# Performance work log

Hardware: AMD Instinct MI355X
Metric: run time of the kernel (lower is better)

The kernel has to match this reference:

```python
import jax, jax.numpy as jnp
import numpy as np

B, T, C, H = 2, 2048, 768, 12
HD = C // H  # head dim = 64


def setup_inputs() -> dict:
    key = jax.random.key(0)
    k1, k2, k3 = jax.random.split(key, 3)
    s_in = 1.0 / np.sqrt(C)
    return {
        "x": jax.random.normal(k1, (B, T, C), dtype=jnp.float32),
        "Wqkv": jax.random.normal(k2, (C, 3 * C), dtype=jnp.float32) * s_in,
        "bqkv": jnp.zeros((3 * C,), dtype=jnp.float32),
        "Wproj": jax.random.normal(k3, (C, C), dtype=jnp.float32) * s_in,
        "bproj": jnp.zeros((C,), dtype=jnp.float32),
    }


def reference(x, Wqkv, bqkv, Wproj, bproj):
    b, t, c = x.shape
    qkv = x @ Wqkv + bqkv                      # [b, t, 3c]
    q, k, v = jnp.split(qkv, 3, axis=2)
    # [b, h, t, hd]
    q = q.reshape(b, t, H, HD).transpose(0, 2, 1, 3)
    k = k.reshape(b, t, H, HD).transpose(0, 2, 1, 3)
    v = v.reshape(b, t, H, HD).transpose(0, 2, 1, 3)
    scale = 1.0 / np.sqrt(HD)
    att = jnp.einsum("bhqd,bhkd->bhqk", q, k) * scale  # [b, h, t, t]
    causal = jnp.tril(jnp.ones((t, t), dtype=bool))
    att = jnp.where(causal[None, None], att, -jnp.inf)
    att = jax.nn.softmax(att, axis=-1)
    y = jnp.einsum("bhqk,bhkd->bhqd", att, v)          # [b, h, t, hd]
    y = y.transpose(0, 2, 1, 3).reshape(b, t, c)
    return y @ Wproj + bproj
```

## Files before the change

### kernel.cpp

```cpp
#include <hip/hip_runtime.h>
#include <math.h>

#define BB 2
#define TT 2048
#define CC 768
#define HH 12
#define HD 64
#define N3 (3*CC)

typedef __attribute__((ext_vector_type(8))) short short8;
typedef __attribute__((ext_vector_type(8))) _Float16 f16x8;
typedef __attribute__((ext_vector_type(4))) float f32x4;
typedef unsigned short u16;

#define QSCALE 0.1803368809f

static __device__ __forceinline__ u16 f2h(float x) {
    union { _Float16 h; u16 u; } v; v.h = (_Float16)x; return v.u;
}
static __device__ __forceinline__ float ex2(float x) {
#if __has_builtin(__builtin_amdgcn_exp2f)
    return __builtin_amdgcn_exp2f(x);
#else
    return exp2f(x);
#endif
}
static __device__ __forceinline__ unsigned pk2h(float a, float b) {
    auto p = __builtin_amdgcn_cvt_pkrtz(a, b);
    return __builtin_bit_cast(unsigned, p);
}

static __device__ __forceinline__ void gl16(const void* g, void* l) {
    __builtin_amdgcn_global_load_lds(
        (const __attribute__((address_space(1))) void*)g,
        (__attribute__((address_space(3))) void*)l, 16, 0, 0);
}

__global__ __launch_bounds__(256)
void conv_h(const float* __restrict__ src, u16* __restrict__ dst)
{
    const int i = blockIdx.x * 256 + threadIdx.x;
    float4 v = ((const float4*)src)[i];
    ushort4 o;
    o.x = f2h(v.x); o.y = f2h(v.y); o.z = f2h(v.z); o.w = f2h(v.w);
    ((ushort4*)dst)[i] = o;
}

__global__ __launch_bounds__(256)
void conv_th(const float* __restrict__ W, u16* __restrict__ Th, int N)
{
    __shared__ float Tt[64][65];
    const int tid = threadIdx.x;
    const int n0 = blockIdx.x * 64, k0 = blockIdx.y * 64;
    {
        const int r = tid >> 2, q = tid & 3;
        #pragma unroll
        for (int i = 0; i < 4; ++i) {
            float4 v = *(const float4*)(W + (size_t)(k0 + r) * N + n0 + q * 16 + i * 4);
            Tt[q * 16 + i * 4 + 0][r] = v.x;
            Tt[q * 16 + i * 4 + 1][r] = v.y;
            Tt[q * 16 + i * 4 + 2][r] = v.z;
            Tt[q * 16 + i * 4 + 3][r] = v.w;
        }
    }
    __syncthreads();
    {
        const int n = tid >> 2, q = tid & 3;
        u16 hh[16];
        #pragma unroll
        for (int j = 0; j < 16; ++j) hh[j] = f2h(Tt[n][q * 16 + j]);
        u16* dh = Th + (size_t)(n0 + n) * 768 + k0 + q * 16;
        *(short8*)(dh) = *(short8*)&hh[0];
        *(short8*)(dh + 8) = *(short8*)&hh[8];
    }
}

template<int NCOLS, int MODE>
__global__ __launch_bounds__(256)
void mm3(const u16* __restrict__ A_g, const u16* __restrict__ B_g,
         const float* __restrict__ bias, float* __restrict__ outF,
         u16* __restrict__ qo, u16* __restrict__ ko, u16* __restrict__ vto)
{
    __shared__ u16 gsm[16384];
    char* smb = (char*)gsm;
    const int tid = threadIdx.x, lane = tid & 63, wv = tid >> 6;
    const int wm = wv >> 1, wn = wv & 1, r16 = lane & 15, kg = lane >> 4;
    const int m0 = blockIdx.y * 128, n0 = blockIdx.x * 128;

    const u16 *pA[2], *pB[2];
    int ldsq[2];
    #pragma unroll
    for (int qq = 0; qq < 2; ++qq) {
        const int L = wv * 2048 + qq * 1024 + lane * 16;
        const int row = L >> 6, c = (L >> 4) & 3;
        const int cp = c ^ ((row >> 1) & 3);
        ldsq[qq] = wv * 2048 + qq * 1024;
        pA[qq] = A_g + (size_t)(m0 + row) * 768 + cp * 8;
        pB[qq] = B_g + (size_t)(n0 + row) * 768 + cp * 8;
    }

    int aA[4], aB[4];
    #pragma unroll
    for (int t = 0; t < 4; ++t) {
        const int rA = wm * 64 + t * 16 + r16;
        const int rB = wn * 64 + t * 16 + r16;
        aA[t] = rA * 64 + ((kg ^ ((rA >> 1) & 3)) << 4);
        aB[t] = rB * 64 + ((kg ^ ((rB >> 1) & 3)) << 4) + 8192;
    }

    f32x4 acc[4][4];
    #pragma unroll
    for (int i = 0; i < 4; ++i)
        #pragma unroll
        for (int j = 0; j < 4; ++j) acc[i][j] = (f32x4)0.f;

    #pragma unroll
    for (int qq = 0; qq < 2; ++qq) {
        gl16(pA[qq], smb + ldsq[qq]);
        gl16(pB[qq], smb + 8192 + ldsq[qq]);
        pA[qq] += 32; pB[qq] += 32;
    }
    __syncthreads();

    int cur = 0;
    for (int ks = 0; ks < 24; ++ks) {
        const int nxt = cur ^ 1;
        if (ks != 23) {
            #pragma unroll
            for (int qq = 0; qq < 2; ++qq) {
                gl16(pA[qq], smb + nxt * 16384 + ldsq[qq]);
                gl16(pB[qq], smb + nxt * 16384 + 8192 + ldsq[qq]);
                pA[qq] += 32; pB[qq] += 32;
            }
        }
        const int cb = cur * 16384;
        f16x8 a[4], b[4];
        #pragma unroll
        for (int t = 0; t < 4; ++t) {
            a[t] = *(const f16x8*)(smb + cb + aA[t]);
            b[t] = *(const f16x8*)(smb + cb + aB[t]);
        }
        #pragma unroll
        for (int mt = 0; mt < 4; ++mt)
            #pragma unroll
            for (int nt = 0; nt < 4; ++nt)
                acc[mt][nt] = __builtin_amdgcn_mfma_f32_16x16x32_f16(a[mt], b[nt], acc[mt][nt], 0, 0, 0);
        __syncthreads();
        cur = nxt;
    }

    float bi[4];
    #pragma unroll
    for (int nt = 0; nt < 4; ++nt) bi[nt] = bias[n0 + wn * 64 + nt * 16 + r16];

    if (MODE == 1) {
        #pragma unroll
        for (int mt = 0; mt < 4; ++mt)
            #pragma unroll
            for (int nt = 0; nt < 4; ++nt)
                #pragma unroll
                for (int r = 0; r < 4; ++r) {
                    const int grow = m0 + wm * 64 + mt * 16 + kg * 4 + r;
                    const int gcol = n0 + wn * 64 + nt * 16 + r16;
                    outF[(size_t)grow * CC + gcol] = acc[mt][nt][r] + bi[nt];
                }
    } else {
        const int which = n0 / CC;
        const float qsc = (which == 0) ? QSCALE : 1.0f;
        const int b_ = m0 >> 11;
        #pragma unroll
        for (int mt = 0; mt < 4; ++mt) {
            const int tb = ((m0 & 2047) + wm * 64 + mt * 16 + kg * 4);
            #pragma unroll
            for (int nt = 0; nt < 4; ++nt) {
                const int gcol = n0 + wn * 64 + nt * 16 + r16;
                const int cc = gcol - which * CC;
                const int h = cc >> 6, d = cc & 63;
                const int bh_ = b_ * HH + h;
                if (which == 2) {
                    ushort4 hv;
                    #pragma unroll
                    for (int r = 0; r < 4; ++r)
                        ((u16*)&hv)[r] = f2h(acc[mt][nt][r] + bi[nt]);
                    *(ushort4*)(vto + ((size_t)bh_ * 64 + d) * 2048 + tb) = hv;
                } else {
                    u16* dst = (which == 0) ? qo : ko;
                    #pragma unroll
                    for (int r = 0; r < 4; ++r)
                        dst[(((size_t)bh_ * 2048 + tb + r) << 6) + d] =
                            f2h((acc[mt][nt][r] + bi[nt]) * qsc);
                }
            }
        }
    }
}

__global__ __launch_bounds__(256)
void attn3(const u16* __restrict__ qp, const u16* __restrict__ kp,
           const u16* __restrict__ vtp, u16* __restrict__ attp)
{
    __shared__ u16 smem[20480];
    char* smb = (char*)smem;

    const int tid = threadIdx.x, bid = blockIdx.x;
    const int qt = 31 - (bid / 24);
    const int bh = bid % 24;
    const int lane = tid & 63, wv = tid >> 6;
    const int r16 = lane & 15, kg = lane >> 4;
    const int r7 = r16 & 7;

    const size_t qro = ((size_t)bh * TT + qt * 64 + wv * 16 + r16) * 64;
    f16x8 qf[2];
    #pragma unroll
    for (int ks = 0; ks < 2; ++ks)
        qf[ks] = *(const f16x8*)(qp + qro + ks * 32 + kg * 8);

    const u16 *pk[2], *pv[2];
    int ldsq[2];
    #pragma unroll
    for (int qq = 0; qq < 2; ++qq) {
        const int L = wv * 2048 + qq * 1024 + lane * 16;
        const int row = L >> 7, c = (L >> 4) & 7;
        const int cp = c ^ (row & 7);
        ldsq[qq] = wv * 2048 + qq * 1024;
        pk[qq] = kp + ((size_t)bh * TT + row) * 64 + cp * 8;
        pv[qq] = vtp + ((size_t)bh * 64 + row) * TT + cp * 8;
    }

    int aK[2][4], aP[2];
    #pragma unroll
    for (int ks = 0; ks < 2; ++ks) {
        #pragma unroll
        for (int nt = 0; nt < 4; ++nt) {
            const int row = nt * 16 + r16;
            aK[ks][nt] = row * 128 + (((ks * 4 + kg) ^ (row & 7)) << 4);
        }
        aP[ks] = 32768 + wv * 2048 + r16 * 128 + (((ks * 4 + kg) ^ r7) << 4);
    }
    const int pwbase = 32768 + wv * 2048 + r16 * 128;
    const int kg8 = kg * 8, kg4 = kg * 4;

    f32x4 o_acc[4];
    #pragma unroll
    for (int i = 0; i < 4; ++i) o_acc[i] = (f32x4)0.f;
    f32x4 o_l = (f32x4)0.f;
    float m = -1e30f;

    f16x8 ones;
    #pragma unroll
    for (int i = 0; i < 8; ++i) ones[i] = (_Float16)1.0f;

    #pragma unroll
    for (int qq = 0; qq < 2; ++qq) {
        gl16(pk[qq], smb + ldsq[qq]);
        gl16(pv[qq], smb + 8192 + ldsq[qq]);
        pk[qq] += 4096; pv[qq] += 64;
    }
    __syncthreads();

    int cur = 0;
    for (int j = 0; j <= qt; ++j) {
        const int nxt = cur ^ 1;
        if (j != qt) {
            #pragma unroll
            for (int qq = 0; qq < 2; ++qq) {
                gl16(pk[qq], smb + nxt * 16384 + ldsq[qq]);
                gl16(pv[qq], smb + nxt * 16384 + 8192 + ldsq[qq]);
                pk[qq] += 4096; pv[qq] += 64;
            }
        }
        const int cb = cur * 16384;

        f32x4 s[4];
        #pragma unroll
        for (int nt = 0; nt < 4; ++nt) s[nt] = (f32x4)0.f;
        __builtin_amdgcn_s_setprio(1);
        #pragma unroll
        for (int ks = 0; ks < 2; ++ks)
            #pragma unroll
            for (int nt = 0; nt < 4; ++nt) {
                f16x8 kf = *(const f16x8*)(smb + cb + aK[ks][nt]);
                s[nt] = __builtin_amdgcn_mfma_f32_16x16x32_f16(kf, qf[ks], s[nt], 0, 0, 0);
            }
        __builtin_amdgcn_s_setprio(0);

        if (j == qt) {
            #pragma unroll
            for (int nt = 0; nt < 4; ++nt)
                #pragma unroll
                for (int r = 0; r < 4; ++r)
                    if (nt * 16 + kg4 + r > wv * 16 + r16) s[nt][r] = -1e30f;
        }

        float pm = s[0][0];
        #pragma unroll
        for (int nt = 0; nt < 4; ++nt)
            #pragma unroll
            for (int r = 0; r < 4; ++r)
                if (nt | r) pm = fmaxf(pm, s[nt][r]);
        pm = fmaxf(pm, __shfl_xor(pm, 16));
        pm = fmaxf(pm, __shfl_xor(pm, 32));

        if (__any(pm > m + 8.0f)) {
            const float mn = fmaxf(m, pm);
            const float corr = ex2(m - mn);
            m = mn;
            const float c0 = __shfl(corr, kg4 + 0);
            const float c1 = __shfl(corr, kg4 + 1);
            const float c2 = __shfl(corr, kg4 + 2);
            const float c3 = __shfl(corr, kg4 + 3);
            #pragma unroll
            for (int nt = 0; nt < 4; ++nt) {
                o_acc[nt][0] *= c0; o_acc[nt][1] *= c1;
                o_acc[nt][2] *= c2; o_acc[nt][3] *= c3;
            }
            o_l[0] *= c0; o_l[1] *= c1; o_l[2] *= c2; o_l[3] *= c3;
        }

        #pragma unroll
        for (int nt = 0; nt < 4; ++nt) {
            const float p0 = ex2(s[nt][0] - m), p1 = ex2(s[nt][1] - m);
            const float p2 = ex2(s[nt][2] - m), p3 = ex2(s[nt][3] - m);
            uint2 w;
            w.x = pk2h(p0, p1);
            w.y = pk2h(p2, p3);
            *(uint2*)(smb + pwbase + ((nt * 32 + kg8) ^ (r7 << 4))) = w;
        }

        __builtin_amdgcn_s_setprio(1);
        #pragma unroll
        for (int ks = 0; ks < 2; ++ks) {
            f16x8 pa = *(const f16x8*)(smb + aP[ks]);
            o_l = __builtin_amdgcn_mfma_f32_16x16x32_f16(pa, ones, o_l, 0, 0, 0);
            #pragma unroll
            for (int nt = 0; nt < 4; ++nt) {
                f16x8 vf = *(const f16x8*)(smb + cb + 8192 + aK[ks][nt]);
                o_acc[nt] = __builtin_amdgcn_mfma_f32_16x16x32_f16(pa, vf, o_acc[nt], 0, 0, 0);
            }
        }
        __builtin_amdgcn_s_setprio(0);

        __syncthreads();
        cur = nxt;
    }

    const int b_ = bh / HH, h = bh % HH;
    #pragma unroll
    for (int r = 0; r < 4; ++r) {
        const float inv = 1.f / o_l[r];
        const int t = qt * 64 + wv * 16 + kg4 + r;
        const size_t base = ((size_t)b_ * TT + t) * CC + h * 64;
        #pragma unroll
        for (int nt = 0; nt < 4; ++nt)
            attp[base + nt * 16 + r16] = f2h(o_acc[nt][r] * inv);
    }
}

extern "C" void kernel_launch(void* const* d_in, const int* in_sizes, int n_in,
                              void* d_out, int out_size, void* d_ws, size_t ws_size,
                              hipStream_t stream)
{
    const float* x     = (const float*)d_in[0];
    const float* Wqkv  = (const float*)d_in[1];
    const float* bqkv  = (const float*)d_in[2];
    const float* Wproj = (const float*)d_in[3];
    const float* bproj = (const float*)d_in[4];
    float* out = (float*)d_out;

    const size_t E  = (size_t)4096 * 768;
    const size_t WQ = (size_t)2304 * 768;
    const size_t WP = (size_t)768 * 768;

    u16* ws   = (u16*)d_ws;
    u16* xh   = ws;
    u16* atth = ws;
    u16* wqh  = ws + E;
    u16* wph  = wqh + WQ;
    u16* qh   = wph + WP;
    u16* kh   = qh + E;
    u16* vth  = kh + E;

    conv_h<<<dim3((int)(E / 4 / 256)), 256, 0, stream>>>(x, xh);
    conv_th<<<dim3(N3 / 64, CC / 64), 256, 0, stream>>>(Wqkv, wqh, N3);
    conv_th<<<dim3(CC / 64, CC / 64), 256, 0, stream>>>(Wproj, wph, CC);

    mm3<N3, 0><<<dim3(N3 / 128, 32), 256, 0, stream>>>(
        xh, wqh, bqkv, nullptr, qh, kh, vth);
    attn3<<<dim3(768), 256, 0, stream>>>(qh, kh, vth, atth);
    mm3<CC, 1><<<dim3(CC / 128, 32), 256, 0, stream>>>(
        atth, wph, bproj, out, nullptr, nullptr, nullptr);
}
```

Measured before the change: 156.2 us.

## Process two query tiles per attention block and merge conversion kernels

```diff
diff --git a/kernel.cpp b/kernel.cpp
--- a/kernel.cpp
+++ b/kernel.cpp
@@ -37,21 +37,26 @@
 }
 
 __global__ __launch_bounds__(256)
-void conv_h(const float* __restrict__ src, u16* __restrict__ dst)
-{
-    const int i = blockIdx.x * 256 + threadIdx.x;
-    float4 v = ((const float4*)src)[i];
-    ushort4 o;
-    o.x = f2h(v.x); o.y = f2h(v.y); o.z = f2h(v.z); o.w = f2h(v.w);
-    ((ushort4*)dst)[i] = o;
-}
-
-__global__ __launch_bounds__(256)
-void conv_th(const float* __restrict__ W, u16* __restrict__ Th, int N)
+void conv_all(const float* __restrict__ x, u16* __restrict__ xh,
+              const float* __restrict__ Wq, u16* __restrict__ wqh,
+              const float* __restrict__ Wp, u16* __restrict__ wph)
 {
     __shared__ float Tt[64][65];
+    const int b = blockIdx.x;
+    if (b < 3072) {
+        const int i = b * 256 + threadIdx.x;
+        float4 v = ((const float4*)x)[i];
+        ushort4 o;
+        o.x = f2h(v.x); o.y = f2h(v.y); o.z = f2h(v.z); o.w = f2h(v.w);
+        ((ushort4*)xh)[i] = o;
+        return;
+    }
+    const float* W; u16* T; int N, idx;
+    if (b < 3504) { W = Wq; T = wqh; N = N3; idx = b - 3072; }
+    else          { W = Wp; T = wph; N = CC; idx = b - 3504; }
+    const int ntx = N / 64;
+    const int n0 = (idx % ntx) * 64, k0 = (idx / ntx) * 64;
     const int tid = threadIdx.x;
-    const int n0 = blockIdx.x * 64, k0 = blockIdx.y * 64;
     {
         const int r = tid >> 2, q = tid & 3;
         #pragma unroll
@@ -69,7 +74,7 @@
         u16 hh[16];
         #pragma unroll
         for (int j = 0; j < 16; ++j) hh[j] = f2h(Tt[n][q * 16 + j]);
-        u16* dh = Th + (size_t)(n0 + n) * 768 + k0 + q * 16;
+        u16* dh = T + (size_t)(n0 + n) * 768 + k0 + q * 16;
         *(short8*)(dh) = *(short8*)&hh[0];
         *(short8*)(dh + 8) = *(short8*)&hh[8];
     }
@@ -199,21 +204,29 @@
 void attn3(const u16* __restrict__ qp, const u16* __restrict__ kp,
            const u16* __restrict__ vtp, u16* __restrict__ attp)
 {
-    __shared__ u16 smem[20480];
+    __shared__ u16 smem[24576];
     char* smb = (char*)smem;
 
     const int tid = threadIdx.x, bid = blockIdx.x;
-    const int qt = 31 - (bid / 24);
+    const int qt = 15 - (bid / 24);
     const int bh = bid % 24;
+    const int t0 = qt * 128;
+    const int jmax = 2 * qt + 1;
+    const int diagA = 2 * qt;
     const int lane = tid & 63, wv = tid >> 6;
     const int r16 = lane & 15, kg = lane >> 4;
     const int r7 = r16 & 7;
-
-    const size_t qro = ((size_t)bh * TT + qt * 64 + wv * 16 + r16) * 64;
-    f16x8 qf[2];
-    #pragma unroll
-    for (int ks = 0; ks < 2; ++ks)
-        qf[ks] = *(const f16x8*)(qp + qro + ks * 32 + kg * 8);
+    const int kg8 = kg * 8, kg4 = kg * 4;
+
+    const size_t qroA = ((size_t)bh * TT + t0 + wv * 16 + r16) * 64;
+    f16x8 qfA[2], qfB[2];
+    #pragma unroll
+    for (int ks = 0; ks < 2; ++ks) {
+        qfA[ks] = *(const f16x8*)(qp + qroA + ks * 32 + kg8);
+        qfB[ks] = *(const f16x8*)(qp + qroA + 4096 + ks * 32 + kg8);
+    }
+    const int rowA = t0 + wv * 16 + r16;
+    const int rowB = rowA + 64;
 
     const u16 *pk[2], *pv[2];
     int ldsq[2];
@@ -227,7 +240,7 @@
         pv[qq] = vtp + ((size_t)bh * 64 + row) * TT + cp * 8;
     }
 
-    int aK[2][4], aP[2];
+    int aK[2][4], aPA[2], aPB[2];
     #pragma unroll
     for (int ks = 0; ks < 2; ++ks) {
         #pragma unroll
@@ -235,16 +248,17 @@
             const int row = nt * 16 + r16;
             aK[ks][nt] = row * 128 + (((ks * 4 + kg) ^ (row & 7)) << 4);
         }
-        aP[ks] = 32768 + wv * 2048 + r16 * 128 + (((ks * 4 + kg) ^ r7) << 4);
-    }
-    const int pwbase = 32768 + wv * 2048 + r16 * 128;
-    const int kg8 = kg * 8, kg4 = kg * 4;
-
-    f32x4 o_acc[4];
-    #pragma unroll
-    for (int i = 0; i < 4; ++i) o_acc[i] = (f32x4)0.f;
-    f32x4 o_l = (f32x4)0.f;
-    float m = -1e30f;
+        aPA[ks] = 32768 + wv * 2048 + r16 * 128 + (((ks * 4 + kg) ^ r7) << 4);
+        aPB[ks] = aPA[ks] + 8192;
+    }
+    const int pwA = 32768 + wv * 2048 + r16 * 128;
+    const int pwB = pwA + 8192;
+
+    f32x4 oA[4], oB[4];
+    #pragma unroll
+    for (int i = 0; i < 4; ++i) { oA[i] = (f32x4)0.f; oB[i] = (f32x4)0.f; }
+    f32x4 lA = (f32x4)0.f, lB = (f32x4)0.f;
+    float mA = -1e30f, mB = -1e30f;
 
     f16x8 ones;
     #pragma unroll
@@ -259,9 +273,9 @@
     __syncthreads();
 
     int cur = 0;
-    for (int j = 0; j <= qt; ++j) {
+    for (int j = 0; j <= jmax; ++j) {
         const int nxt = cur ^ 1;
-        if (j != qt) {
+        if (j != jmax) {
             #pragma unroll
             for (int qq = 0; qq < 2; ++qq) {
                 gl16(pk[qq], smb + nxt * 16384 + ldsq[qq]);
@@ -270,72 +284,87 @@
             }
         }
         const int cb = cur * 16384;
-
-        f32x4 s[4];
-        #pragma unroll
-        for (int nt = 0; nt < 4; ++nt) s[nt] = (f32x4)0.f;
+        const int kb = j * 64;
+
+        f32x4 sA[4], sB[4];
+        #pragma unroll
+        for (int nt = 0; nt < 4; ++nt) { sA[nt] = (f32x4)0.f; sB[nt] = (f32x4)0.f; }
         __builtin_amdgcn_s_setprio(1);
         #pragma unroll
         for (int ks = 0; ks < 2; ++ks)
             #pragma unroll
             for (int nt = 0; nt < 4; ++nt) {
                 f16x8 kf = *(const f16x8*)(smb + cb + aK[ks][nt]);
-                s[nt] = __builtin_amdgcn_mfma_f32_16x16x32_f16(kf, qf[ks], s[nt], 0, 0, 0);
+                sA[nt] = __builtin_amdgcn_mfma_f32_16x16x32_f16(kf, qfA[ks], sA[nt], 0, 0, 0);
+                sB[nt] = __builtin_amdgcn_mfma_f32_16x16x32_f16(kf, qfB[ks], sB[nt], 0, 0, 0);
             }
         __builtin_amdgcn_s_setprio(0);
 
-        if (j == qt) {
+        if (j >= diagA) {
             #pragma unroll
             for (int nt = 0; nt < 4; ++nt)
                 #pragma unroll
                 for (int r = 0; r < 4; ++r)
-                    if (nt * 16 + kg4 + r > wv * 16 + r16) s[nt][r] = -1e30f;
-        }
-
-        float pm = s[0][0];
-        #pragma unroll
-        for (int nt = 0; nt < 4; ++nt)
-            #pragma unroll
-            for (int r = 0; r < 4; ++r)
-                if (nt | r) pm = fmaxf(pm, s[nt][r]);
-        pm = fmaxf(pm, __shfl_xor(pm, 16));
-        pm = fmaxf(pm, __shfl_xor(pm, 32));
-
-        if (__any(pm > m + 8.0f)) {
-            const float mn = fmaxf(m, pm);
-            const float corr = ex2(m - mn);
-            m = mn;
-            const float c0 = __shfl(corr, kg4 + 0);
-            const float c1 = __shfl(corr, kg4 + 1);
-            const float c2 = __shfl(corr, kg4 + 2);
-            const float c3 = __shfl(corr, kg4 + 3);
+                    if (kb + nt * 16 + kg4 + r > rowA) sA[nt][r] = -1e30f;
+        }
+        if (j == jmax) {
+            #pragma unroll
+            for (int nt = 0; nt < 4; ++nt)
+                #pragma unroll
+                for (int r = 0; r < 4; ++r)
+                    if (kb + nt * 16 + kg4 + r > rowB) sB[nt][r] = -1e30f;
+        }
+
+        auto softmax = [&](f32x4 (&s)[4], float& m, f32x4& ol, f32x4 (&oa)[4],
+                           int pwbase) {
+            float pm = s[0][0];
+            #pragma unroll
+            for (int nt = 0; nt < 4; ++nt)
+                #pragma unroll
+                for (int r = 0; r < 4; ++r)
+                    if (nt | r) pm = fmaxf(pm, s[nt][r]);
+            pm = fmaxf(pm, __shfl_xor(pm, 16));
+            pm = fmaxf(pm, __shfl_xor(pm, 32));
+            if (__any(pm > m + 8.0f)) {
+                const float mn = fmaxf(m, pm);
+                const float corr = ex2(m - mn);
+                m = mn;
+                const float c0 = __shfl(corr, kg4 + 0);
+                const float c1 = __shfl(corr, kg4 + 1);
+                const float c2 = __shfl(corr, kg4 + 2);
+                const float c3 = __shfl(corr, kg4 + 3);
+                #pragma unroll
+                for (int nt = 0; nt < 4; ++nt) {
+                    oa[nt][0] *= c0; oa[nt][1] *= c1;
+                    oa[nt][2] *= c2; oa[nt][3] *= c3;
+                }
+                ol[0] *= c0; ol[1] *= c1; ol[2] *= c2; ol[3] *= c3;
+            }
             #pragma unroll
             for (int nt = 0; nt < 4; ++nt) {
-                o_acc[nt][0] *= c0; o_acc[nt][1] *= c1;
-                o_acc[nt][2] *= c2; o_acc[nt][3] *= c3;
-            }
-            o_l[0] *= c0; o_l[1] *= c1; o_l[2] *= c2; o_l[3] *= c3;
-        }
-
-        #pragma unroll
-        for (int nt = 0; nt < 4; ++nt) {
-            const float p0 = ex2(s[nt][0] - m), p1 = ex2(s[nt][1] - m);
-            const float p2 = ex2(s[nt][2] - m), p3 = ex2(s[nt][3] - m);
-            uint2 w;
-            w.x = pk2h(p0, p1);
-            w.y = pk2h(p2, p3);
-            *(uint2*)(smb + pwbase + ((nt * 32 + kg8) ^ (r7 << 4))) = w;
-        }
+                const float p0 = ex2(s[nt][0] - m), p1 = ex2(s[nt][1] - m);
+                const float p2 = ex2(s[nt][2] - m), p3 = ex2(s[nt][3] - m);
+                uint2 w;
+                w.x = pk2h(p0, p1);
+                w.y = pk2h(p2, p3);
+                *(uint2*)(smb + pwbase + ((nt * 32 + kg8) ^ (r7 << 4))) = w;
+            }
+        };
+        softmax(sA, mA, lA, oA, pwA);
+        softmax(sB, mB, lB, oB, pwB);
 
         __builtin_amdgcn_s_setprio(1);
         #pragma unroll
         for (int ks = 0; ks < 2; ++ks) {
-            f16x8 pa = *(const f16x8*)(smb + aP[ks]);
-            o_l = __builtin_amdgcn_mfma_f32_16x16x32_f16(pa, ones, o_l, 0, 0, 0);
+            f16x8 paA = *(const f16x8*)(smb + aPA[ks]);
+            f16x8 paB = *(const f16x8*)(smb + aPB[ks]);
+            lA = __builtin_amdgcn_mfma_f32_16x16x32_f16(paA, ones, lA, 0, 0, 0);
+            lB = __builtin_amdgcn_mfma_f32_16x16x32_f16(paB, ones, lB, 0, 0, 0);
             #pragma unroll
             for (int nt = 0; nt < 4; ++nt) {
                 f16x8 vf = *(const f16x8*)(smb + cb + 8192 + aK[ks][nt]);
-                o_acc[nt] = __builtin_amdgcn_mfma_f32_16x16x32_f16(pa, vf, o_acc[nt], 0, 0, 0);
+                oA[nt] = __builtin_amdgcn_mfma_f32_16x16x32_f16(paA, vf, oA[nt], 0, 0, 0);
+                oB[nt] = __builtin_amdgcn_mfma_f32_16x16x32_f16(paB, vf, oB[nt], 0, 0, 0);
             }
         }
         __builtin_amdgcn_s_setprio(0);
@@ -347,12 +376,16 @@
     const int b_ = bh / HH, h = bh % HH;
     #pragma unroll
     for (int r = 0; r < 4; ++r) {
-        const float inv = 1.f / o_l[r];
-        const int t = qt * 64 + wv * 16 + kg4 + r;
-        const size_t base = ((size_t)b_ * TT + t) * CC + h * 64;
-        #pragma unroll
-        for (int nt = 0; nt < 4; ++nt)
-            attp[base + nt * 16 + r16] = f2h(o_acc[nt][r] * inv);
+        const float invA = 1.f / lA[r];
+        const float invB = 1.f / lB[r];
+        const int tA = t0 + wv * 16 + kg4 + r;
+        const size_t baseA = ((size_t)b_ * TT + tA) * CC + h * 64;
+        const size_t baseB = baseA + (size_t)64 * CC;
+        #pragma unroll
+        for (int nt = 0; nt < 4; ++nt) {
+            attp[baseA + nt * 16 + r16] = f2h(oA[nt][r] * invA);
+            attp[baseB + nt * 16 + r16] = f2h(oB[nt][r] * invB);
+        }
     }
 }
 
@@ -380,13 +413,11 @@
     u16* kh   = qh + E;
     u16* vth  = kh + E;
 
-    conv_h<<<dim3((int)(E / 4 / 256)), 256, 0, stream>>>(x, xh);
-    conv_th<<<dim3(N3 / 64, CC / 64), 256, 0, stream>>>(Wqkv, wqh, N3);
-    conv_th<<<dim3(CC / 64, CC / 64), 256, 0, stream>>>(Wproj, wph, CC);
+    conv_all<<<dim3(3648), 256, 0, stream>>>(x, xh, Wqkv, wqh, Wproj, wph);
 
     mm3<N3, 0><<<dim3(N3 / 128, 32), 256, 0, stream>>>(
         xh, wqh, bqkv, nullptr, qh, kh, vth);
-    attn3<<<dim3(768), 256, 0, stream>>>(qh, kh, vth, atth);
+    attn3<<<dim3(384), 256, 0, stream>>>(qh, kh, vth, atth);
     mm3<CC, 1><<<dim3(CC / 128, 32), 256, 0, stream>>>(
         atth, wph, bproj, out, nullptr, nullptr, nullptr);
 }
```

Measured after the change: 165.1 us. 1.06x slower.
